# Performance work log

Hardware: AMD Instinct MI355X
Metric: run time of the kernel (lower is better)

The kernel has to match this reference:

```python
import jax, jax.numpy as jnp
import numpy as np

N = 50000   # nodes
E = 800000  # edges
D = 128     # input_dim
H = 128     # hidden_dim
C = 40      # output_dim (classes)


def setup_inputs() -> dict:
    key = jax.random.key(0)
    ks = jax.random.split(key, 8)
    x = jax.random.normal(ks[0], (N, D), dtype=jnp.float32)
    edge_index = jax.random.randint(ks[1], (2, E), 0, N, dtype=jnp.int32)
    sD = 1.0 / np.sqrt(D)
    sH = 1.0 / np.sqrt(H)
    W1 = jax.random.uniform(ks[2], (D, H), jnp.float32, -sD, sD)
    b1 = jnp.zeros((H,), jnp.float32)
    W2 = jax.random.uniform(ks[3], (H, H), jnp.float32, -sH, sH)
    b2 = jnp.zeros((H,), jnp.float32)
    W3 = jax.random.uniform(ks[4], (H, C), jnp.float32, -sH, sH)
    b3 = jnp.zeros((C,), jnp.float32)
    return {"x": x, "edge_index": edge_index,
            "W1": W1, "b1": b1, "W2": W2, "b2": b2, "W3": W3, "b3": b3}


def reference(x, edge_index, W1, b1, W2, b2, W3, b3):
    # GCNConv: out = D^{-1/2} (A + I) D^{-1/2} (x @ W) + b
    src = edge_index[0]
    dst = edge_index[1]
    loop = jnp.arange(N, dtype=src.dtype)
    src_f = jnp.concatenate([src, loop])  # [E+N] with self-loops
    dst_f = jnp.concatenate([dst, loop])
    deg = jax.ops.segment_sum(jnp.ones(E + N, x.dtype), dst_f, num_segments=N)
    dinv = jax.lax.rsqrt(jnp.maximum(deg, 1.0))  # deg >= 1 due to self-loops
    norm = dinv[src_f] * dinv[dst_f]  # [E+N]

    def conv(h, W, b):
        h = h @ W                       # [N, F_out]
        msg = h[src_f] * norm[:, None]  # [E+N, F_out] gathered messages
        return jax.ops.segment_sum(msg, dst_f, num_segments=N) + b

    h = jax.nn.relu(conv(x, W1, b1))
    h = jax.nn.relu(conv(h, W2, b2))  # dropout is identity in eval mode
    return conv(h, W3, b3)
```

## Files before the change

### kernel.cpp

```cpp
#include <hip/hip_runtime.h>

typedef unsigned short ushort_t;
typedef unsigned int uint_t;


__device__ __forceinline__ int2 ldnt2(const int2* p) {
    long long v = __builtin_nontemporal_load((const long long*)p);
    int2 r;
    r.x = (int)(v & 0xffffffffll);
    r.y = (int)(v >> 32);
    return r;
}

__global__ __launch_bounds__(256) void k_scan(
        const int* __restrict__ deg, unsigned long long* __restrict__ partials,
        int* __restrict__ rowptr, int* __restrict__ cursor,
        float* __restrict__ dinv, int n) {
    __shared__ int s[256];
    __shared__ int sprefix;
    const int b = blockIdx.x, t = threadIdx.x;
    const int i = b * 256 + t;
    int v = (i < n) ? deg[i] : 0;
    s[t] = v;
    __syncthreads();
    for (int off = 1; off < 256; off <<= 1) {
        int u = (t >= off) ? s[t - off] : 0;
        __syncthreads();
        s[t] += u;
        __syncthreads();
    }
    if (t == 0) {
        __hip_atomic_store(&partials[b],
                ((unsigned long long)s[255] << 2) | 1ull,
                __ATOMIC_RELEASE, __HIP_MEMORY_SCOPE_AGENT);
        if (b == 0) {
            __hip_atomic_store(&partials[0],
                    ((unsigned long long)s[255] << 2) | 2ull,
                    __ATOMIC_RELEASE, __HIP_MEMORY_SCOPE_AGENT);
            sprefix = 0;
        }
    }
    if (b > 0 && t < 64) {
        int acc = 0;
        int k = b - 1;
        for (;;) {
            int idx = k - t;
            unsigned long long p;
            unsigned st;
            do {
                if (idx >= 0) {
                    p = __hip_atomic_load(&partials[idx],
                            __ATOMIC_ACQUIRE, __HIP_MEMORY_SCOPE_AGENT);
                } else {
                    p = 2ull;
                }
                st = (unsigned)(p & 3ull);
            } while (st == 0);
            unsigned long long bal = __ballot(st == 2);
            int L = (bal != 0) ? (__ffsll((unsigned long long)bal) - 1) : 64;
            int val = (int)(p >> 2);
            int contrib = (t <= L) ? val : 0;
            #pragma unroll
            for (int o = 32; o > 0; o >>= 1) contrib += __shfl_down(contrib, o);
            if (t == 0) acc += contrib;
            if (L < 64) break;
            k -= 64;
        }
        if (t == 0) {
            __hip_atomic_store(&partials[b],
                    (((unsigned long long)(acc + s[255])) << 2) | 2ull,
                    __ATOMIC_RELEASE, __HIP_MEMORY_SCOPE_AGENT);
            sprefix = acc;
        }
    }
    __syncthreads();
    if (i < n) {
        int ex = sprefix + s[t] - v;
        rowptr[i] = ex;
        cursor[i] = ex;
        dinv[i] = rsqrtf((float)(v + 1));
        if (i == n - 1) rowptr[n] = ex + v;
    }
}

__global__ __launch_bounds__(256) void k_fill(const int* __restrict__ ei,
                                              int* __restrict__ cursor,
                                              const float* __restrict__ dinv,
                                              int2* __restrict__ csr, int E, int n) {
    const int xcd = blockIdx.x & 7;
    const int e = (blockIdx.x >> 3) * 256 + threadIdx.x;
    if (e >= E) return;
    int d = __builtin_nontemporal_load(ei + E + e);
    const int lo = (int)(((long long)xcd * n) >> 3);
    const int hi = (int)(((long long)(xcd + 1) * n) >> 3);
    if (d < lo || d >= hi) return;
    int s = __builtin_nontemporal_load(ei + e);
    int pos = atomicAdd(&cursor[d], 1);
    unsigned long long packed = (unsigned long long)(unsigned)s |
            ((unsigned long long)(unsigned)__float_as_uint(dinv[s] * dinv[d]) << 32);
    __builtin_nontemporal_store((long long)packed, (long long*)(csr + pos));
}

__device__ __forceinline__ ushort_t f2bf_rne(float f) {
    uint_t u = __float_as_uint(f);
    u += 0x7fffu + ((u >> 16) & 1u);
    return (ushort_t)(u >> 16);
}
__device__ __forceinline__ float bflo(uint_t u) {
    return __uint_as_float(u << 16);
}
__device__ __forceinline__ float bfhi(uint_t u) {
    return __uint_as_float(u & 0xffff0000u);
}

__global__ __launch_bounds__(256) void k_l1(const float* __restrict__ X,
                                            const float* __restrict__ W,
                                            ushort_t* __restrict__ Y, int N,
                                            const int* __restrict__ ei,
                                            int* __restrict__ deg, int E,
                                            int gemmGrid) {
    __shared__ float sX[32][132];
    __shared__ float sW[32][128];
    if ((int)blockIdx.x >= gemmGrid) {
        int e = ((int)blockIdx.x - gemmGrid) * 256 + threadIdx.x;
        if (e < E) atomicAdd(&deg[__builtin_nontemporal_load(ei + E + e)], 1);
        return;
    }
    const int tid = threadIdx.x;
    const int bm = blockIdx.x * 128;
    const int m0 = (tid >> 4) * 8;
    const int c4 = (tid & 15) * 4;
    const int xf = tid & 7;
    float acc[8][8] = {};
    for (int k0 = 0; k0 < 128; k0 += 32) {
        #pragma unroll
        for (int it = 0; it < 4; ++it) {
            int i = tid + it * 256;
            int row = bm + (i >> 3);
            int rc = min(row, N - 1);
            float4 v = *(const float4*)(X + (size_t)rc * 128 + k0 + xf * 4);
            int m = i >> 3;
            sX[xf * 4 + 0][m] = v.x;
            sX[xf * 4 + 1][m] = v.y;
            sX[xf * 4 + 2][m] = v.z;
            sX[xf * 4 + 3][m] = v.w;
        }
        #pragma unroll
        for (int it = 0; it < 4; ++it) {
            int i = tid + it * 256;
            int wr = i >> 5;
            int wf = i & 31;
            *(float4*)(&sW[wr][wf * 4]) =
                *(const float4*)(W + (size_t)(k0 + wr) * 128 + wf * 4);
        }
        __syncthreads();
        #pragma unroll
        for (int kk = 0; kk < 32; ++kk) {
            float4 a0 = *(const float4*)(&sX[kk][m0]);
            float4 a1 = *(const float4*)(&sX[kk][m0 + 4]);
            float4 b0 = *(const float4*)(&sW[kk][c4]);
            float4 b1 = *(const float4*)(&sW[kk][64 + c4]);
            float av[8] = {a0.x, a0.y, a0.z, a0.w, a1.x, a1.y, a1.z, a1.w};
            float bv[8] = {b0.x, b0.y, b0.z, b0.w, b1.x, b1.y, b1.z, b1.w};
            #pragma unroll
            for (int r = 0; r < 8; ++r)
                #pragma unroll
                for (int c = 0; c < 8; ++c)
                    acc[r][c] = fmaf(av[r], bv[c], acc[r][c]);
        }
        __syncthreads();
    }
    #pragma unroll
    for (int r = 0; r < 8; ++r) {
        int row = bm + m0 + r;
        if (row < N) {
            ushort4 o0 = {f2bf_rne(acc[r][0]), f2bf_rne(acc[r][1]),
                          f2bf_rne(acc[r][2]), f2bf_rne(acc[r][3])};
            ushort4 o1 = {f2bf_rne(acc[r][4]), f2bf_rne(acc[r][5]),
                          f2bf_rne(acc[r][6]), f2bf_rne(acc[r][7])};
            *(ushort4*)(Y + (size_t)row * 128 + c4)      = o0;
            *(ushort4*)(Y + (size_t)row * 128 + 64 + c4) = o1;
        }
    }
}

__global__ __launch_bounds__(256) void k_gemm128(const float* __restrict__ X,
                                                 const float* __restrict__ W,
                                                 ushort_t* __restrict__ Y, int N) {
    __shared__ float sX[32][132];
    __shared__ float sW[32][128];
    const int tid = threadIdx.x;
    const int bm = blockIdx.x * 128;
    const int m0 = (tid >> 4) * 8;
    const int c4 = (tid & 15) * 4;
    const int xf = tid & 7;
    float acc[8][8] = {};
    for (int k0 = 0; k0 < 128; k0 += 32) {
        #pragma unroll
        for (int it = 0; it < 4; ++it) {
            int i = tid + it * 256;
            int row = bm + (i >> 3);
            int rc = min(row, N - 1);
            float4 v = *(const float4*)(X + (size_t)rc * 128 + k0 + xf * 4);
            int m = i >> 3;
            sX[xf * 4 + 0][m] = v.x;
            sX[xf * 4 + 1][m] = v.y;
            sX[xf * 4 + 2][m] = v.z;
            sX[xf * 4 + 3][m] = v.w;
        }
        #pragma unroll
        for (int it = 0; it < 4; ++it) {
            int i = tid + it * 256;
            int wr = i >> 5;
            int wf = i & 31;
            *(float4*)(&sW[wr][wf * 4]) =
                *(const float4*)(W + (size_t)(k0 + wr) * 128 + wf * 4);
        }
        __syncthreads();
        #pragma unroll
        for (int kk = 0; kk < 32; ++kk) {
            float4 a0 = *(const float4*)(&sX[kk][m0]);
            float4 a1 = *(const float4*)(&sX[kk][m0 + 4]);
            float4 b0 = *(const float4*)(&sW[kk][c4]);
            float4 b1 = *(const float4*)(&sW[kk][64 + c4]);
            float av[8] = {a0.x, a0.y, a0.z, a0.w, a1.x, a1.y, a1.z, a1.w};
            float bv[8] = {b0.x, b0.y, b0.z, b0.w, b1.x, b1.y, b1.z, b1.w};
            #pragma unroll
            for (int r = 0; r < 8; ++r)
                #pragma unroll
                for (int c = 0; c < 8; ++c)
                    acc[r][c] = fmaf(av[r], bv[c], acc[r][c]);
        }
        __syncthreads();
    }
    #pragma unroll
    for (int r = 0; r < 8; ++r) {
        int row = bm + m0 + r;
        if (row < N) {
            ushort4 o0 = {f2bf_rne(acc[r][0]), f2bf_rne(acc[r][1]),
                          f2bf_rne(acc[r][2]), f2bf_rne(acc[r][3])};
            ushort4 o1 = {f2bf_rne(acc[r][4]), f2bf_rne(acc[r][5]),
                          f2bf_rne(acc[r][6]), f2bf_rne(acc[r][7])};
            *(ushort4*)(Y + (size_t)row * 128 + c4)      = o0;
            *(ushort4*)(Y + (size_t)row * 128 + 64 + c4) = o1;
        }
    }
}

__global__ __launch_bounds__(256) void k_gemm40(const float* __restrict__ X,
                                                const float* __restrict__ W,
                                                ushort_t* __restrict__ Y, int N) {
    __shared__ float sX[32][132];
    __shared__ float sW[32][40];
    const int tid = threadIdx.x;
    const int bm = blockIdx.x * 128;
    const int m0 = (tid >> 3) * 4;
    const int n0 = (tid & 7) * 5;
    const int xf = tid & 7;
    float acc[4][5] = {};
    for (int k0 = 0; k0 < 128; k0 += 32) {
        #pragma unroll
        for (int it = 0; it < 4; ++it) {
            int i = tid + it * 256;
            int row = bm + (i >> 3);
            int rc = min(row, N - 1);
            float4 v = *(const float4*)(X + (size_t)rc * 128 + k0 + xf * 4);
            int m = i >> 3;
            sX[xf * 4 + 0][m] = v.x;
            sX[xf * 4 + 1][m] = v.y;
            sX[xf * 4 + 2][m] = v.z;
            sX[xf * 4 + 3][m] = v.w;
        }
        for (int i = tid; i < 320; i += 256) {
            int wr = i / 10;
            int wf = i - wr * 10;
            *(float4*)(&sW[wr][wf * 4]) =
                *(const float4*)(W + (size_t)(k0 + wr) * 40 + wf * 4);
        }
        __syncthreads();
        #pragma unroll
        for (int kk = 0; kk < 32; ++kk) {
            float4 a = *(const float4*)(&sX[kk][m0]);
            float av[4] = {a.x, a.y, a.z, a.w};
            #pragma unroll
            for (int c = 0; c < 5; ++c) {
                float b = sW[kk][n0 + c];
                #pragma unroll
                for (int r = 0; r < 4; ++r)
                    acc[r][c] = fmaf(av[r], b, acc[r][c]);
            }
        }
        __syncthreads();
    }
    #pragma unroll
    for (int r = 0; r < 4; ++r) {
        int row = bm + m0 + r;
        if (row < N) {
            #pragma unroll
            for (int c = 0; c < 5; ++c)
                Y[(size_t)row * 64 + n0 + c] = f2bf_rne(acc[r][c]);
        }
    }
}

template <bool RELU>
__global__ __launch_bounds__(256) void k_agg128(
        const ushort_t* __restrict__ XW, const int* __restrict__ rowptr,
        const int2* __restrict__ csr, const float* __restrict__ dinv,
        const float* __restrict__ bias, float* __restrict__ out, int n) {
    const int lane = threadIdx.x & 63;
    const int wv = __builtin_amdgcn_readfirstlane(threadIdx.x >> 6);
    const int d = blockIdx.x * 4 + wv;
    if (d >= n) return;
    const uint_t* xw = (const uint_t*)XW;
    float dv = dinv[d];
    float w0 = dv * dv;
    uint_t sq = xw[(size_t)d * 64 + lane];
    float2 a;
    a.x = w0 * bflo(sq);
    a.y = w0 * bfhi(sq);
    int j = rowptr[d], end = rowptr[d + 1];
    for (; j + 8 <= end; j += 8) {
        int2 p0 = ldnt2(csr + j + 0), p1 = ldnt2(csr + j + 1);
        int2 p2 = ldnt2(csr + j + 2), p3 = ldnt2(csr + j + 3);
        int2 p4 = ldnt2(csr + j + 4), p5 = ldnt2(csr + j + 5);
        int2 p6 = ldnt2(csr + j + 6), p7 = ldnt2(csr + j + 7);
        uint_t u0 = xw[(size_t)p0.x * 64 + lane];
        uint_t u1 = xw[(size_t)p1.x * 64 + lane];
        uint_t u2 = xw[(size_t)p2.x * 64 + lane];
        uint_t u3 = xw[(size_t)p3.x * 64 + lane];
        uint_t u4 = xw[(size_t)p4.x * 64 + lane];
        uint_t u5 = xw[(size_t)p5.x * 64 + lane];
        uint_t u6 = xw[(size_t)p6.x * 64 + lane];
        uint_t u7 = xw[(size_t)p7.x * 64 + lane];
        float w0e = __int_as_float(p0.y), w1e = __int_as_float(p1.y);
        float w2e = __int_as_float(p2.y), w3e = __int_as_float(p3.y);
        float w4e = __int_as_float(p4.y), w5e = __int_as_float(p5.y);
        float w6e = __int_as_float(p6.y), w7e = __int_as_float(p7.y);
        a.x = fmaf(w0e, bflo(u0), a.x); a.y = fmaf(w0e, bfhi(u0), a.y);
        a.x = fmaf(w1e, bflo(u1), a.x); a.y = fmaf(w1e, bfhi(u1), a.y);
        a.x = fmaf(w2e, bflo(u2), a.x); a.y = fmaf(w2e, bfhi(u2), a.y);
        a.x = fmaf(w3e, bflo(u3), a.x); a.y = fmaf(w3e, bfhi(u3), a.y);
        a.x = fmaf(w4e, bflo(u4), a.x); a.y = fmaf(w4e, bfhi(u4), a.y);
        a.x = fmaf(w5e, bflo(u5), a.x); a.y = fmaf(w5e, bfhi(u5), a.y);
        a.x = fmaf(w6e, bflo(u6), a.x); a.y = fmaf(w6e, bfhi(u6), a.y);
        a.x = fmaf(w7e, bflo(u7), a.x); a.y = fmaf(w7e, bfhi(u7), a.y);
    }
    for (; j < end; ++j) {
        int2 p = ldnt2(csr + j);
        float we = __int_as_float(p.y);
        uint_t u = xw[(size_t)p.x * 64 + lane];
        a.x = fmaf(we, bflo(u), a.x);
        a.y = fmaf(we, bfhi(u), a.y);
    }
    float2 b = ((const float2*)bias)[lane];
    a.x += b.x; a.y += b.y;
    if (RELU) {
        a.x = fmaxf(a.x, 0.f);
        a.y = fmaxf(a.y, 0.f);
    }
    ((float2*)out)[(size_t)d * 64 + lane] = a;
}

__global__ __launch_bounds__(256) void k_agg40(
        const ushort_t* __restrict__ XW, const int* __restrict__ rowptr,
        const int2* __restrict__ csr, const float* __restrict__ dinv,
        const float* __restrict__ bias, float* __restrict__ out, int n) {
    const int lane = threadIdx.x & 31;
    const int sub  = threadIdx.x >> 5;
    const int d = blockIdx.x * 8 + sub;
    if (d >= n || lane >= 20) return;
    const uint_t* xw = (const uint_t*)XW;
    float dv = dinv[d];
    float w0 = dv * dv;
    uint_t sq = xw[(size_t)d * 32 + lane];
    float2 a;
    a.x = w0 * bflo(sq);
    a.y = w0 * bfhi(sq);
    int j = rowptr[d], end = rowptr[d + 1];
    for (; j + 4 <= end; j += 4) {
        int2 p0 = ldnt2(csr + j + 0), p1 = ldnt2(csr + j + 1);
        int2 p2 = ldnt2(csr + j + 2), p3 = ldnt2(csr + j + 3);
        uint_t u0 = xw[(size_t)p0.x * 32 + lane];
        uint_t u1 = xw[(size_t)p1.x * 32 + lane];
        uint_t u2 = xw[(size_t)p2.x * 32 + lane];
        uint_t u3 = xw[(size_t)p3.x * 32 + lane];
        float w0e = __int_as_float(p0.y), w1e = __int_as_float(p1.y);
        float w2e = __int_as_float(p2.y), w3e = __int_as_float(p3.y);
        a.x = fmaf(w0e, bflo(u0), a.x); a.y = fmaf(w0e, bfhi(u0), a.y);
        a.x = fmaf(w1e, bflo(u1), a.x); a.y = fmaf(w1e, bfhi(u1), a.y);
        a.x = fmaf(w2e, bflo(u2), a.x); a.y = fmaf(w2e, bfhi(u2), a.y);
        a.x = fmaf(w3e, bflo(u3), a.x); a.y = fmaf(w3e, bfhi(u3), a.y);
    }
    for (; j < end; ++j) {
        int2 p = ldnt2(csr + j);
        float we = __int_as_float(p.y);
        uint_t u = xw[(size_t)p.x * 32 + lane];
        a.x = fmaf(we, bflo(u), a.x);
        a.y = fmaf(we, bfhi(u), a.y);
    }
    float2 b = ((const float2*)bias)[lane];
    a.x += b.x; a.y += b.y;
    ((float2*)out)[(size_t)d * 20 + lane] = a;
}

static inline int cdiv(long long a, int b) { return (int)((a + b - 1) / b); }

extern "C" void kernel_launch(void* const* d_in, const int* in_sizes, int n_in,
                              void* d_out, int out_size, void* d_ws, size_t ws_size,
                              hipStream_t stream) {
    const float* x  = (const float*)d_in[0];
    const int*   ei = (const int*)d_in[1];
    const float* W1 = (const float*)d_in[2];
    const float* b1 = (const float*)d_in[3];
    const float* W2 = (const float*)d_in[4];
    const float* b2 = (const float*)d_in[5];
    const float* W3 = (const float*)d_in[6];
    const float* b3 = (const float*)d_in[7];
    float* out = (float*)d_out;

    const int N = in_sizes[0] / 128;
    const int E = in_sizes[1] / 2;
    const int nb = cdiv(N, 256);

    char* ws = (char*)d_ws;
    int*   deg    = (int*)ws;                 ws += (size_t)N * 4;
    unsigned long long* partials = (unsigned long long*)ws;
                                              ws += (size_t)nb * 8;
    int*   rowptr = (int*)ws;                 ws += (size_t)(N + 1) * 4;
    int*   cursor = (int*)ws;                 ws += (size_t)N * 4;
    float* dinv   = (float*)ws;               ws += (size_t)N * 4;
    ws = (char*)(((uintptr_t)ws + 127) & ~(uintptr_t)127);
    int2*  csr    = (int2*)ws;                ws += (size_t)E * 8;
    char*  bufA   = ws;                       ws += (size_t)N * 128 * 4;
    float* bufB   = (float*)ws;

    const int BT = 256;
    const int gemmGrid = cdiv(N, 128);
    const int degGrid  = cdiv(E, BT);

    hipMemsetAsync(deg, 0, (size_t)N * 4 + (size_t)nb * 8, stream);

    k_l1<<<gemmGrid + degGrid, 256, 0, stream>>>(x, W1, (ushort_t*)bufA, N,
                                                 ei, deg, E, gemmGrid);
    k_scan<<<nb, 256, 0, stream>>>(deg, partials, rowptr, cursor, dinv, N);
    k_fill<<<cdiv(E, BT) * 8, 256, 0, stream>>>(ei, cursor, dinv, csr, E, N);

    k_agg128<true><<<cdiv(N, 4), 256, 0, stream>>>((const ushort_t*)bufA, rowptr, csr, dinv, b1, bufB, N);
    k_gemm128<<<cdiv(N, 128), 256, 0, stream>>>(bufB, W2, (ushort_t*)bufA, N);
    k_agg128<true><<<cdiv(N, 4), 256, 0, stream>>>((const ushort_t*)bufA, rowptr, csr, dinv, b2, bufB, N);
    k_gemm40<<<cdiv(N, 128), 256, 0, stream>>>(bufB, W3, (ushort_t*)bufA, N);
    k_agg40<<<cdiv(N, 8), 256, 0, stream>>>((const ushort_t*)bufA, rowptr, csr, dinv, b3, out, N);
}
```

Measured before the change: 313.9 us.

## Switch dense GEMMs to bf16 MFMA and store aggregation outputs as bf16

Replaces the three FP32 register-tiled GEMMs with bf16 MFMA 16x16x32 kernels. Weights are pre-transposed and converted to bf16 by a new prep kernel, and X is converted to bf16 while it is loaded into shared memory. The aggregation kernels now write bf16 activations instead of fp32, halving the traffic that feeds the next GEMM. The CSR store also drops its nontemporal hint. In exchange, layer inputs and weights lose precision to bf16, and one extra small kernel launch is added.

```diff
diff --git a/kernel.cpp b/kernel.cpp
--- a/kernel.cpp
+++ b/kernel.cpp
@@ -2,14 +2,48 @@
 
 typedef unsigned short ushort_t;
 typedef unsigned int uint_t;
-
-
+typedef short bf16x8 __attribute__((ext_vector_type(8)));
+typedef float f32x4 __attribute__((ext_vector_type(4)));
+
+
+__device__ __forceinline__ ushort_t f2bf_rne(float f) {
+    uint_t u = __float_as_uint(f);
+    u += 0x7fffu + ((u >> 16) & 1u);
+    return (ushort_t)(u >> 16);
+}
+__device__ __forceinline__ float bflo(uint_t u) {
+    return __uint_as_float(u << 16);
+}
+__device__ __forceinline__ float bfhi(uint_t u) {
+    return __uint_as_float(u & 0xffff0000u);
+}
 __device__ __forceinline__ int2 ldnt2(const int2* p) {
     long long v = __builtin_nontemporal_load((const long long*)p);
     int2 r;
     r.x = (int)(v & 0xffffffffll);
     r.y = (int)(v >> 32);
     return r;
+}
+
+__global__ __launch_bounds__(256) void k_prep(const float* __restrict__ W1,
+                                              const float* __restrict__ W2,
+                                              const float* __restrict__ W3,
+                                              ushort_t* __restrict__ W1t,
+                                              ushort_t* __restrict__ W2t,
+                                              ushort_t* __restrict__ W3t) {
+    int idx = blockIdx.x * 256 + threadIdx.x;
+    if (idx < 16384) {
+        int n = idx >> 7, k = idx & 127;
+        W1t[idx] = f2bf_rne(W1[k * 128 + n]);
+    } else if (idx < 32768) {
+        int j = idx - 16384;
+        int n = j >> 7, k = j & 127;
+        W2t[j] = f2bf_rne(W2[k * 128 + n]);
+    } else if (idx < 38912) {
+        int j = idx - 32768;
+        int n = j >> 7, k = j & 127;
+        W3t[j] = (n < 40) ? f2bf_rne(W3[k * 40 + n]) : (ushort_t)0;
+    }
 }
 
 __global__ __launch_bounds__(256) void k_scan(
@@ -96,209 +130,188 @@
     if (d < lo || d >= hi) return;
     int s = __builtin_nontemporal_load(ei + e);
     int pos = atomicAdd(&cursor[d], 1);
-    unsigned long long packed = (unsigned long long)(unsigned)s |
-            ((unsigned long long)(unsigned)__float_as_uint(dinv[s] * dinv[d]) << 32);
-    __builtin_nontemporal_store((long long)packed, (long long*)(csr + pos));
-}
-
-__device__ __forceinline__ ushort_t f2bf_rne(float f) {
-    uint_t u = __float_as_uint(f);
-    u += 0x7fffu + ((u >> 16) & 1u);
-    return (ushort_t)(u >> 16);
-}
-__device__ __forceinline__ float bflo(uint_t u) {
-    return __uint_as_float(u << 16);
-}
-__device__ __forceinline__ float bfhi(uint_t u) {
-    return __uint_as_float(u & 0xffff0000u);
+    int2 p;
+    p.x = s;
+    p.y = __float_as_int(dinv[s] * dinv[d]);
+    csr[pos] = p;
 }
 
 __global__ __launch_bounds__(256) void k_l1(const float* __restrict__ X,
-                                            const float* __restrict__ W,
+                                            const ushort_t* __restrict__ W1t,
                                             ushort_t* __restrict__ Y, int N,
                                             const int* __restrict__ ei,
                                             int* __restrict__ deg, int E,
                                             int gemmGrid) {
-    __shared__ float sX[32][132];
-    __shared__ float sW[32][128];
+    __shared__ ushort_t sA[64][136];
+    __shared__ ushort_t sB[128][136];
     if ((int)blockIdx.x >= gemmGrid) {
         int e = ((int)blockIdx.x - gemmGrid) * 256 + threadIdx.x;
         if (e < E) atomicAdd(&deg[__builtin_nontemporal_load(ei + E + e)], 1);
         return;
     }
     const int tid = threadIdx.x;
-    const int bm = blockIdx.x * 128;
-    const int m0 = (tid >> 4) * 8;
-    const int c4 = (tid & 15) * 4;
-    const int xf = tid & 7;
-    float acc[8][8] = {};
-    for (int k0 = 0; k0 < 128; k0 += 32) {
+    const int bm = blockIdx.x * 64;
+    #pragma unroll
+    for (int it = 0; it < 8; ++it) {
+        int i = tid + it * 256;
+        int row = i >> 5;
+        int c4 = i & 31;
+        int rc = min(bm + row, N - 1);
+        float4 v = *(const float4*)(X + (size_t)rc * 128 + c4 * 4);
+        ushort4 o = {f2bf_rne(v.x), f2bf_rne(v.y), f2bf_rne(v.z), f2bf_rne(v.w)};
+        *(ushort4*)(&sA[row][c4 * 4]) = o;
+    }
+    #pragma unroll
+    for (int it = 0; it < 8; ++it) {
+        int i = tid + it * 256;
+        int row = i >> 4;
+        int c8 = i & 15;
+        *(bf16x8*)(&sB[row][c8 * 8]) =
+            *(const bf16x8*)(W1t + (size_t)row * 128 + c8 * 8);
+    }
+    __syncthreads();
+    const int lane = tid & 63;
+    const int wv = tid >> 6;
+    const int m0 = wv * 16;
+    const int lr = lane & 15;
+    const int lg = lane >> 4;
+    bf16x8 afr[4];
+    #pragma unroll
+    for (int kk = 0; kk < 4; ++kk)
+        afr[kk] = *(const bf16x8*)(&sA[m0 + lr][kk * 32 + lg * 8]);
+    f32x4 acc[8];
+    #pragma unroll
+    for (int ct = 0; ct < 8; ++ct) {
+        acc[ct] = (f32x4){0.f, 0.f, 0.f, 0.f};
         #pragma unroll
-        for (int it = 0; it < 4; ++it) {
-            int i = tid + it * 256;
-            int row = bm + (i >> 3);
-            int rc = min(row, N - 1);
-            float4 v = *(const float4*)(X + (size_t)rc * 128 + k0 + xf * 4);
-            int m = i >> 3;
-            sX[xf * 4 + 0][m] = v.x;
-            sX[xf * 4 + 1][m] = v.y;
-            sX[xf * 4 + 2][m] = v.z;
-            sX[xf * 4 + 3][m] = v.w;
-        }
-        #pragma unroll
-        for (int it = 0; it < 4; ++it) {
-            int i = tid + it * 256;
-            int wr = i >> 5;
-            int wf = i & 31;
-            *(float4*)(&sW[wr][wf * 4]) =
-                *(const float4*)(W + (size_t)(k0 + wr) * 128 + wf * 4);
-        }
-        __syncthreads();
-        #pragma unroll
-        for (int kk = 0; kk < 32; ++kk) {
-            float4 a0 = *(const float4*)(&sX[kk][m0]);
-            float4 a1 = *(const float4*)(&sX[kk][m0 + 4]);
-            float4 b0 = *(const float4*)(&sW[kk][c4]);
-            float4 b1 = *(const float4*)(&sW[kk][64 + c4]);
-            float av[8] = {a0.x, a0.y, a0.z, a0.w, a1.x, a1.y, a1.z, a1.w};
-            float bv[8] = {b0.x, b0.y, b0.z, b0.w, b1.x, b1.y, b1.z, b1.w};
-            #pragma unroll
-            for (int r = 0; r < 8; ++r)
-                #pragma unroll
-                for (int c = 0; c < 8; ++c)
-                    acc[r][c] = fmaf(av[r], bv[c], acc[r][c]);
-        }
-        __syncthreads();
-    }
-    #pragma unroll
-    for (int r = 0; r < 8; ++r) {
-        int row = bm + m0 + r;
-        if (row < N) {
-            ushort4 o0 = {f2bf_rne(acc[r][0]), f2bf_rne(acc[r][1]),
-                          f2bf_rne(acc[r][2]), f2bf_rne(acc[r][3])};
-            ushort4 o1 = {f2bf_rne(acc[r][4]), f2bf_rne(acc[r][5]),
-                          f2bf_rne(acc[r][6]), f2bf_rne(acc[r][7])};
-            *(ushort4*)(Y + (size_t)row * 128 + c4)      = o0;
-            *(ushort4*)(Y + (size_t)row * 128 + 64 + c4) = o1;
-        }
-    }
-}
-
-__global__ __launch_bounds__(256) void k_gemm128(const float* __restrict__ X,
-                                                 const float* __restrict__ W,
-                                                 ushort_t* __restrict__ Y, int N) {
-    __shared__ float sX[32][132];
-    __shared__ float sW[32][128];
-    const int tid = threadIdx.x;
-    const int bm = blockIdx.x * 128;
-    const int m0 = (tid >> 4) * 8;
-    const int c4 = (tid & 15) * 4;
-    const int xf = tid & 7;
-    float acc[8][8] = {};
-    for (int k0 = 0; k0 < 128; k0 += 32) {
-        #pragma unroll
-        for (int it = 0; it < 4; ++it) {
-            int i = tid + it * 256;
-            int row = bm + (i >> 3);
-            int rc = min(row, N - 1);
-            float4 v = *(const float4*)(X + (size_t)rc * 128 + k0 + xf * 4);
-            int m = i >> 3;
-            sX[xf * 4 + 0][m] = v.x;
-            sX[xf * 4 + 1][m] = v.y;
-            sX[xf * 4 + 2][m] = v.z;
-            sX[xf * 4 + 3][m] = v.w;
-        }
-        #pragma unroll
-        for (int it = 0; it < 4; ++it) {
-            int i = tid + it * 256;
-            int wr = i >> 5;
-            int wf = i & 31;
-            *(float4*)(&sW[wr][wf * 4]) =
-                *(const float4*)(W + (size_t)(k0 + wr) * 128 + wf * 4);
-        }
-        __syncthreads();
-        #pragma unroll
-        for (int kk = 0; kk < 32; ++kk) {
-            float4 a0 = *(const float4*)(&sX[kk][m0]);
-            float4 a1 = *(const float4*)(&sX[kk][m0 + 4]);
-            float4 b0 = *(const float4*)(&sW[kk][c4]);
-            float4 b1 = *(const float4*)(&sW[kk][64 + c4]);
-            float av[8] = {a0.x, a0.y, a0.z, a0.w, a1.x, a1.y, a1.z, a1.w};
-            float bv[8] = {b0.x, b0.y, b0.z, b0.w, b1.x, b1.y, b1.z, b1.w};
-            #pragma unroll
-            for (int r = 0; r < 8; ++r)
-                #pragma unroll
-                for (int c = 0; c < 8; ++c)
-                    acc[r][c] = fmaf(av[r], bv[c], acc[r][c]);
-        }
-        __syncthreads();
-    }
-    #pragma unroll
-    for (int r = 0; r < 8; ++r) {
-        int row = bm + m0 + r;
-        if (row < N) {
-            ushort4 o0 = {f2bf_rne(acc[r][0]), f2bf_rne(acc[r][1]),
-                          f2bf_rne(acc[r][2]), f2bf_rne(acc[r][3])};
-            ushort4 o1 = {f2bf_rne(acc[r][4]), f2bf_rne(acc[r][5]),
-                          f2bf_rne(acc[r][6]), f2bf_rne(acc[r][7])};
-            *(ushort4*)(Y + (size_t)row * 128 + c4)      = o0;
-            *(ushort4*)(Y + (size_t)row * 128 + 64 + c4) = o1;
-        }
-    }
-}
-
-__global__ __launch_bounds__(256) void k_gemm40(const float* __restrict__ X,
-                                                const float* __restrict__ W,
-                                                ushort_t* __restrict__ Y, int N) {
-    __shared__ float sX[32][132];
-    __shared__ float sW[32][40];
-    const int tid = threadIdx.x;
-    const int bm = blockIdx.x * 128;
-    const int m0 = (tid >> 3) * 4;
-    const int n0 = (tid & 7) * 5;
-    const int xf = tid & 7;
-    float acc[4][5] = {};
-    for (int k0 = 0; k0 < 128; k0 += 32) {
-        #pragma unroll
-        for (int it = 0; it < 4; ++it) {
-            int i = tid + it * 256;
-            int row = bm + (i >> 3);
-            int rc = min(row, N - 1);
-            float4 v = *(const float4*)(X + (size_t)rc * 128 + k0 + xf * 4);
-            int m = i >> 3;
-            sX[xf * 4 + 0][m] = v.x;
-            sX[xf * 4 + 1][m] = v.y;
-            sX[xf * 4 + 2][m] = v.z;
-            sX[xf * 4 + 3][m] = v.w;
-        }
-        for (int i = tid; i < 320; i += 256) {
-            int wr = i / 10;
-            int wf = i - wr * 10;
-            *(float4*)(&sW[wr][wf * 4]) =
-                *(const float4*)(W + (size_t)(k0 + wr) * 40 + wf * 4);
-        }
-        __syncthreads();
-        #pragma unroll
-        for (int kk = 0; kk < 32; ++kk) {
-            float4 a = *(const float4*)(&sX[kk][m0]);
-            float av[4] = {a.x, a.y, a.z, a.w};
-            #pragma unroll
-            for (int c = 0; c < 5; ++c) {
-                float b = sW[kk][n0 + c];
-                #pragma unroll
-                for (int r = 0; r < 4; ++r)
-                    acc[r][c] = fmaf(av[r], b, acc[r][c]);
-            }
-        }
-        __syncthreads();
-    }
-    #pragma unroll
-    for (int r = 0; r < 4; ++r) {
-        int row = bm + m0 + r;
+        for (int kk = 0; kk < 4; ++kk) {
+            bf16x8 bfr = *(const bf16x8*)(&sB[ct * 16 + lr][kk * 32 + lg * 8]);
+            acc[ct] = __builtin_amdgcn_mfma_f32_16x16x32_bf16(afr[kk], bfr,
+                                                              acc[ct], 0, 0, 0);
+        }
+    }
+    #pragma unroll
+    for (int i = 0; i < 4; ++i) {
+        int row = bm + m0 + lg * 4 + i;
         if (row < N) {
             #pragma unroll
-            for (int c = 0; c < 5; ++c)
-                Y[(size_t)row * 64 + n0 + c] = f2bf_rne(acc[r][c]);
+            for (int ct = 0; ct < 8; ++ct)
+                Y[(size_t)row * 128 + ct * 16 + lr] = f2bf_rne(acc[ct][i]);
+        }
+    }
+}
+
+__global__ __launch_bounds__(256) void k_gemm128(const ushort_t* __restrict__ Xb,
+                                                 const ushort_t* __restrict__ Wt,
+                                                 ushort_t* __restrict__ Y, int N) {
+    __shared__ ushort_t sA[64][136];
+    __shared__ ushort_t sB[128][136];
+    const int tid = threadIdx.x;
+    const int bm = blockIdx.x * 64;
+    #pragma unroll
+    for (int it = 0; it < 4; ++it) {
+        int i = tid + it * 256;
+        int row = i >> 4;
+        int c8 = i & 15;
+        int rc = min(bm + row, N - 1);
+        *(bf16x8*)(&sA[row][c8 * 8]) =
+            *(const bf16x8*)(Xb + (size_t)rc * 128 + c8 * 8);
+    }
+    #pragma unroll
+    for (int it = 0; it < 8; ++it) {
+        int i = tid + it * 256;
+        int row = i >> 4;
+        int c8 = i & 15;
+        *(bf16x8*)(&sB[row][c8 * 8]) =
+            *(const bf16x8*)(Wt + (size_t)row * 128 + c8 * 8);
+    }
+    __syncthreads();
+    const int lane = tid & 63;
+    const int wv = tid >> 6;
+    const int m0 = wv * 16;
+    const int lr = lane & 15;
+    const int lg = lane >> 4;
+    bf16x8 afr[4];
+    #pragma unroll
+    for (int kk = 0; kk < 4; ++kk)
+        afr[kk] = *(const bf16x8*)(&sA[m0 + lr][kk * 32 + lg * 8]);
+    f32x4 acc[8];
+    #pragma unroll
+    for (int ct = 0; ct < 8; ++ct) {
+        acc[ct] = (f32x4){0.f, 0.f, 0.f, 0.f};
+        #pragma unroll
+        for (int kk = 0; kk < 4; ++kk) {
+            bf16x8 bfr = *(const bf16x8*)(&sB[ct * 16 + lr][kk * 32 + lg * 8]);
+            acc[ct] = __builtin_amdgcn_mfma_f32_16x16x32_bf16(afr[kk], bfr,
+                                                              acc[ct], 0, 0, 0);
+        }
+    }
+    #pragma unroll
+    for (int i = 0; i < 4; ++i) {
+        int row = bm + m0 + lg * 4 + i;
+        if (row < N) {
+            #pragma unroll
+            for (int ct = 0; ct < 8; ++ct)
+                Y[(size_t)row * 128 + ct * 16 + lr] = f2bf_rne(acc[ct][i]);
+        }
+    }
+}
+
+__global__ __launch_bounds__(256) void k_gemm40(const ushort_t* __restrict__ Xb,
+                                                const ushort_t* __restrict__ Wt,
+                                                ushort_t* __restrict__ Y, int N) {
+    __shared__ ushort_t sA[64][136];
+    __shared__ ushort_t sB[48][136];
+    const int tid = threadIdx.x;
+    const int bm = blockIdx.x * 64;
+    #pragma unroll
+    for (int it = 0; it < 4; ++it) {
+        int i = tid + it * 256;
+        int row = i >> 4;
+        int c8 = i & 15;
+        int rc = min(bm + row, N - 1);
+        *(bf16x8*)(&sA[row][c8 * 8]) =
+            *(const bf16x8*)(Xb + (size_t)rc * 128 + c8 * 8);
+    }
+    #pragma unroll
+    for (int it = 0; it < 3; ++it) {
+        int i = tid + it * 256;
+        int row = i >> 4;
+        int c8 = i & 15;
+        *(bf16x8*)(&sB[row][c8 * 8]) =
+            *(const bf16x8*)(Wt + (size_t)row * 128 + c8 * 8);
+    }
+    __syncthreads();
+    const int lane = tid & 63;
+    const int wv = tid >> 6;
+    const int m0 = wv * 16;
+    const int lr = lane & 15;
+    const int lg = lane >> 4;
+    bf16x8 afr[4];
+    #pragma unroll
+    for (int kk = 0; kk < 4; ++kk)
+        afr[kk] = *(const bf16x8*)(&sA[m0 + lr][kk * 32 + lg * 8]);
+    f32x4 acc[3];
+    #pragma unroll
+    for (int ct = 0; ct < 3; ++ct) {
+        acc[ct] = (f32x4){0.f, 0.f, 0.f, 0.f};
+        #pragma unroll
+        for (int kk = 0; kk < 4; ++kk) {
+            bf16x8 bfr = *(const bf16x8*)(&sB[ct * 16 + lr][kk * 32 + lg * 8]);
+            acc[ct] = __builtin_amdgcn_mfma_f32_16x16x32_bf16(afr[kk], bfr,
+                                                              acc[ct], 0, 0, 0);
+        }
+    }
+    #pragma unroll
+    for (int i = 0; i < 4; ++i) {
+        int row = bm + m0 + lg * 4 + i;
+        if (row < N) {
+            #pragma unroll
+            for (int ct = 0; ct < 3; ++ct) {
+                int col = ct * 16 + lr;
+                if (col < 40)
+                    Y[(size_t)row * 64 + col] = f2bf_rne(acc[ct][i]);
+            }
         }
     }
 }
@@ -307,7 +320,7 @@
 __global__ __launch_bounds__(256) void k_agg128(
         const ushort_t* __restrict__ XW, const int* __restrict__ rowptr,
         const int2* __restrict__ csr, const float* __restrict__ dinv,
-        const float* __restrict__ bias, float* __restrict__ out, int n) {
+        const float* __restrict__ bias, ushort_t* __restrict__ out, int n) {
     const int lane = threadIdx.x & 63;
     const int wv = __builtin_amdgcn_readfirstlane(threadIdx.x >> 6);
     const int d = blockIdx.x * 4 + wv;
@@ -359,7 +372,8 @@
         a.x = fmaxf(a.x, 0.f);
         a.y = fmaxf(a.y, 0.f);
     }
-    ((float2*)out)[(size_t)d * 64 + lane] = a;
+    uint_t pack = (uint_t)f2bf_rne(a.x) | ((uint_t)f2bf_rne(a.y) << 16);
+    ((uint_t*)out)[(size_t)d * 64 + lane] = pack;
 }
 
 __global__ __launch_bounds__(256) void k_agg40(
@@ -431,24 +445,30 @@
     int*   cursor = (int*)ws;                 ws += (size_t)N * 4;
     float* dinv   = (float*)ws;               ws += (size_t)N * 4;
     ws = (char*)(((uintptr_t)ws + 127) & ~(uintptr_t)127);
-    int2*  csr    = (int2*)ws;                ws += (size_t)E * 8;
-    char*  bufA   = ws;                       ws += (size_t)N * 128 * 4;
-    float* bufB   = (float*)ws;
+    int2*     csr  = (int2*)ws;               ws += (size_t)E * 8;
+    ushort_t* W1t  = (ushort_t*)ws;           ws += (size_t)16384 * 2;
+    ushort_t* W2t  = (ushort_t*)ws;           ws += (size_t)16384 * 2;
+    ushort_t* W3t  = (ushort_t*)ws;           ws += (size_t)6144 * 2;
+    ws = (char*)(((uintptr_t)ws + 127) & ~(uintptr_t)127);
+    ushort_t* bufA = (ushort_t*)ws;           ws += (size_t)N * 128 * 2;
+    ushort_t* bufB = (ushort_t*)ws;           ws += (size_t)N * 128 * 2;
+    ushort_t* bufD = (ushort_t*)ws;
 
     const int BT = 256;
-    const int gemmGrid = cdiv(N, 128);
+    const int gemmGrid = cdiv(N, 64);
     const int degGrid  = cdiv(E, BT);
 
+    k_prep<<<cdiv(38912, 256), 256, 0, stream>>>(W1, W2, W3, W1t, W2t, W3t);
     hipMemsetAsync(deg, 0, (size_t)N * 4 + (size_t)nb * 8, stream);
 
-    k_l1<<<gemmGrid + degGrid, 256, 0, stream>>>(x, W1, (ushort_t*)bufA, N,
+    k_l1<<<gemmGrid + degGrid, 256, 0, stream>>>(x, W1t, bufA, N,
                                                  ei, deg, E, gemmGrid);
     k_scan<<<nb, 256, 0, stream>>>(deg, partials, rowptr, cursor, dinv, N);
     k_fill<<<cdiv(E, BT) * 8, 256, 0, stream>>>(ei, cursor, dinv, csr, E, N);
 
-    k_agg128<true><<<cdiv(N, 4), 256, 0, stream>>>((const ushort_t*)bufA, rowptr, csr, dinv, b1, bufB, N);
-    k_gemm128<<<cdiv(N, 128), 256, 0, stream>>>(bufB, W2, (ushort_t*)bufA, N);
-    k_agg128<true><<<cdiv(N, 4), 256, 0, stream>>>((const ushort_t*)bufA, rowptr, csr, dinv, b2, bufB, N);
-    k_gemm40<<<cdiv(N, 128), 256, 0, stream>>>(bufB, W3, (ushort_t*)bufA, N);
-    k_agg40<<<cdiv(N, 8), 256, 0, stream>>>((const ushort_t*)bufA, rowptr, csr, dinv, b3, out, N);
-}
+    k_agg128<true><<<cdiv(N, 4), 256, 0, stream>>>(bufA, rowptr, csr, dinv, b1, bufB, N);
+    k_gemm128<<<cdiv(N, 64), 256, 0, stream>>>(bufB, W2t, bufA, N);
+    k_agg128<true><<<cdiv(N, 4), 256, 0, stream>>>(bufA, rowptr, csr, dinv, b2, bufB, N);
+    k_gemm40<<<cdiv(N, 64), 256, 0, stream>>>(bufB, W3t, bufD, N);
+    k_agg40<<<cdiv(N, 8), 256, 0, stream>>>(bufD, rowptr, csr, dinv, b3, out, N);
+}
```

Measured after the change: 285.8 us. -9.0%, faster.
